# Kernel tuning notes

Hardware: AMD Instinct MI355X
Metric: run time of the kernel (lower is better)

## Reference

```python
import jax, jax.numpy as jnp
import numpy as np

BS = 2
EMBED = 256
NH = 8
NL = 4
NP = 4
HD = EMBED // NH
SHAPES = [(128, 128), (64, 64), (32, 32), (16, 16)]
NQ = sum(h * w for h, w in SHAPES)  # 21760


def setup_inputs() -> dict:
    key = jax.random.key(0)
    ks = jax.random.split(key, 12)
    s = 1.0 / np.sqrt(EMBED)
    return {
        "query": jax.random.normal(ks[0], (BS, NQ, EMBED), jnp.float32),
        "reference_points": jax.random.uniform(ks[1], (BS, NQ, NL, 2), jnp.float32),
        "value": jax.random.normal(ks[2], (BS, NQ, EMBED), jnp.float32),
        "W_off": jax.random.normal(ks[3], (EMBED, NH * NL * NP * 2), jnp.float32) * 0.01,
        "b_off": jax.random.normal(ks[4], (NH * NL * NP * 2,), jnp.float32) * 0.5,
        "W_attn": jax.random.normal(ks[5], (EMBED, NH * NL * NP), jnp.float32) * 0.02,
        "b_attn": jnp.zeros((NH * NL * NP,), jnp.float32),
        "W_v": jax.random.normal(ks[6], (EMBED, EMBED), jnp.float32) * s,
        "b_v": jnp.zeros((EMBED,), jnp.float32),
        "W_out": jax.random.normal(ks[7], (EMBED, EMBED), jnp.float32) * s,
        "b_out": jnp.zeros((EMBED,), jnp.float32),
        "value_spatial_shapes": np.asarray(SHAPES, dtype=np.int64),
    }


def _ms_deform_attn(value, shapes, loc, aw):
    # value: [bs,V,nh,d]; loc: [bs,nq,nh,L,P,2] in [0,1]; aw: [bs,nq,nh,L,P]
    bs, V, nh, d = value.shape
    nq = loc.shape[1]
    out = jnp.zeros((bs, nq, nh, d), value.dtype)
    start = 0
    b_idx = jnp.arange(bs)[:, None, None, None]
    h_idx = jnp.arange(nh)[None, None, :, None]
    for l, (H, W) in enumerate(shapes):
        H, W = int(H), int(W)
        v = value[:, start:start + H * W].reshape(bs, H, W, nh, d)
        start += H * W
        g = 2.0 * loc[:, :, :, l] - 1.0  # [bs,nq,nh,P,2], grid_sample convention
        # align_corners=False pixel coordinates
        x = ((g[..., 0] + 1.0) * W - 1.0) * 0.5
        y = ((g[..., 1] + 1.0) * H - 1.0) * 0.5
        x0 = jnp.floor(x); y0 = jnp.floor(y)
        wx1 = x - x0; wx0 = 1.0 - wx1
        wy1 = y - y0; wy0 = 1.0 - wy1

        def gather(yi, xi):
            inb = (yi >= 0) & (yi < H) & (xi >= 0) & (xi < W)
            yc = jnp.clip(yi, 0, H - 1).astype(jnp.int32)
            xc = jnp.clip(xi, 0, W - 1).astype(jnp.int32)
            vals = v[b_idx, yc, xc, h_idx]  # [bs,nq,nh,P,d]
            return vals * inb[..., None].astype(v.dtype)

        samp = (gather(y0, x0) * (wy0 * wx0)[..., None]
                + gather(y0, x0 + 1) * (wy0 * wx1)[..., None]
                + gather(y0 + 1, x0) * (wy1 * wx0)[..., None]
                + gather(y0 + 1, x0 + 1) * (wy1 * wx1)[..., None])
        out = out + jnp.einsum('bqhpd,bqhp->bqhd', samp, aw[:, :, :, l])
    return out.reshape(bs, nq, nh * d)


def reference(query, reference_points, value, W_off, b_off, W_attn, b_attn,
              W_v, b_v, W_out, b_out, value_spatial_shapes):
    shapes = np.asarray(value_spatial_shapes)  # static [L,2]
    bs, nq, _ = query.shape
    v = (value @ W_v + b_v).reshape(bs, -1, NH, HD)
    off = (query @ W_off + b_off).reshape(bs, nq, NH, NL, NP, 2)
    aw = (query @ W_attn + b_attn).reshape(bs, nq, NH, NL * NP)
    aw = jax.nn.softmax(aw, axis=-1).reshape(bs, nq, NH, NL, NP)
    # offset normalizer: (W,H) per level
    norm = jnp.asarray(shapes[:, ::-1].astype(np.float32))  # [L,2]
    loc = reference_points[:, :, None, :, None, :] + off / norm[None, None, None, :, None, :]
    out = _ms_deform_attn(v, shapes, loc, aw)
    return out @ W_out + b_out
```

## Files before the change

kernel.cpp:

```cpp
#include <hip/hip_runtime.h>
#include <math.h>

#define BS 2
#define NQ 21760
#define V_LEN 21760
#define EMBED 256
#define NH 8
#define NL 4
#define NP 4
#define HD 32

typedef __bf16 bf16;
typedef __bf16 bf16x8 __attribute__((ext_vector_type(8)));
typedef __bf16 bf16x4 __attribute__((ext_vector_type(4)));
typedef float f32x4 __attribute__((ext_vector_type(4)));
typedef float f32x2 __attribute__((ext_vector_type(2)));
typedef unsigned int u32;

#define GLOAD_LDS16(gp, lp_) \
    __builtin_amdgcn_global_load_lds( \
        (const __attribute__((address_space(1))) unsigned int*)(gp), \
        (__attribute__((address_space(3))) unsigned int*)(lp_), 16, 0, 0)

__global__ __launch_bounds__(256) void cast_all(
    const float* __restrict__ W_v, const float* __restrict__ W_off,
    const float* __restrict__ W_attn, const float* __restrict__ W_out,
    const float* __restrict__ b_off, const float* __restrict__ b_attn,
    bf16* __restrict__ WTv, bf16* __restrict__ WToa, bf16* __restrict__ WTu,
    float* __restrict__ bcat)
{
    const int bid = blockIdx.x;
    if (bid == 896) {
        int id = threadIdx.x;
        if (id < 384) bcat[id] = (id < 256) ? b_off[id] : b_attn[id - 256];
        return;
    }
    int id = bid * 256 + threadIdx.x;
    if (id < 65536) {
        int n = id >> 8, k = id & 255;
        WTv[id] = (bf16)W_v[k * 256 + n];
    } else if (id < 131072) {
        int j = id - 65536; int n = j >> 8, k = j & 255;
        WToa[j] = (bf16)W_off[k * 256 + n];
    } else if (id < 163840) {
        int j = id - 131072; int n = j >> 8, k = j & 255;
        WToa[65536 + j] = (bf16)W_attn[k * 128 + n];
    } else {
        int j = id - 163840; int n = j >> 8, k = j & 255;
        WTu[j] = (bf16)W_out[k * 256 + n];
    }
}

template<bool A_F32, bool OUT_BF16>
__global__ __launch_bounds__(256) void gemm_mfma(
    const void* __restrict__ Av, const bf16* __restrict__ WT,
    const float* __restrict__ bias, void* __restrict__ Cv,
    int N, int K, int ntn)
{
    const int bnt = blockIdx.x % ntn;
    const int bmt = blockIdx.x / ntn;
    const int bm = bmt * 128, bn = bnt * 128;

    __shared__ __align__(16) bf16 Bs[2][128 * 32];
    __shared__ __align__(16) unsigned char AsRaw[2][A_F32 ? 128 * 32 * 4
                                                         : 128 * 32 * 2];

    const int tid = threadIdx.x;
    const int lane = tid & 63, wv = tid >> 6;
    const int wr = wv >> 1, wc = wv & 1;
    const int quad = lane >> 4, l16 = lane & 15;

    f32x4 acc[4][4];
    #pragma unroll
    for (int i = 0; i < 4; i++)
        #pragma unroll
        for (int j = 0; j < 4; j++)
            acc[i][j] = (f32x4){0.f, 0.f, 0.f, 0.f};

    const int b_row = tid >> 2, b_chunk = tid & 3;
    const int a_row8 = tid >> 3, a_phys = tid & 7;
    constexpr int NB = A_F32 ? 6 : 4;

    auto stage = [&](int buf, int k0) {
        if constexpr (A_F32) {
            const float* A = (const float*)Av;
            #pragma unroll
            for (int p = 0; p < 4; p++) {
                int row = a_row8 + p * 32;
                int csrc = a_phys ^ (row & 7);
                GLOAD_LDS16(&A[(size_t)(bm + row) * K + k0 + csrc * 4],
                            &AsRaw[buf][p * 4096 + tid * 16]);
            }
        } else {
            const bf16* A = (const bf16*)Av;
            #pragma unroll
            for (int p = 0; p < 2; p++) {
                int row = b_row + p * 64;
                GLOAD_LDS16(&A[(size_t)(bm + row) * K + k0 + b_chunk * 8],
                            &AsRaw[buf][p * 4096 + tid * 16]);
            }
        }
        #pragma unroll
        for (int p = 0; p < 2; p++) {
            int row = b_row + p * 64;
            GLOAD_LDS16(&WT[(size_t)(bn + row) * K + k0 + b_chunk * 8],
                        (unsigned char*)&Bs[buf][0] + p * 4096 + tid * 16);
        }
    };

    const int nt = K >> 5;
    stage(0, 0);
    int cur = 0;
    for (int t = 0; t < nt; t++) {
        __builtin_amdgcn_s_barrier();
        if (t + 1 < nt) {
            stage(cur ^ 1, (t + 1) << 5);
            asm volatile("s_waitcnt vmcnt(%0)" :: "n"(NB) : "memory");
        } else {
            asm volatile("s_waitcnt vmcnt(0)" ::: "memory");
        }
        __builtin_amdgcn_s_barrier();

        bf16x8 af[4], bfr[4];
        if constexpr (A_F32) {
            const float* Asf = (const float*)&AsRaw[cur][0];
            #pragma unroll
            for (int mi = 0; mi < 4; mi++) {
                int r = wr * 64 + mi * 16 + l16;
                int g = r & 7;
                f32x4 u0 = *(const f32x4*)&Asf[r * 32 + ((2 * quad) ^ g) * 4];
                f32x4 u1 = *(const f32x4*)&Asf[r * 32 + ((2 * quad + 1) ^ g) * 4];
                bf16x8 hh;
                hh[0] = (bf16)u0[0]; hh[1] = (bf16)u0[1]; hh[2] = (bf16)u0[2]; hh[3] = (bf16)u0[3];
                hh[4] = (bf16)u1[0]; hh[5] = (bf16)u1[1]; hh[6] = (bf16)u1[2]; hh[7] = (bf16)u1[3];
                af[mi] = hh;
            }
        } else {
            const bf16* Asb = (const bf16*)&AsRaw[cur][0];
            #pragma unroll
            for (int mi = 0; mi < 4; mi++) {
                int r = wr * 64 + mi * 16 + l16;
                af[mi] = *(const bf16x8*)&Asb[r * 32 + quad * 8];
            }
        }
        #pragma unroll
        for (int ni = 0; ni < 4; ni++) {
            int r = wc * 64 + ni * 16 + l16;
            bfr[ni] = *(const bf16x8*)&Bs[cur][r * 32 + quad * 8];
        }
        #pragma unroll
        for (int mi = 0; mi < 4; mi++)
            #pragma unroll
            for (int ni = 0; ni < 4; ni++)
                acc[mi][ni] = __builtin_amdgcn_mfma_f32_16x16x32_bf16(
                    af[mi], bfr[ni], acc[mi][ni], 0, 0, 0);
        cur ^= 1;
    }

    #pragma unroll
    for (int mi = 0; mi < 4; mi++) {
        #pragma unroll
        for (int ni = 0; ni < 4; ni++) {
            const int col = bn + wc * 64 + ni * 16 + l16;
            const int row0 = bm + wr * 64 + mi * 16 + quad * 4;
            const float bc = bias[col];
            #pragma unroll
            for (int r = 0; r < 4; r++) {
                float v = acc[mi][ni][r] + bc;
                if constexpr (OUT_BF16)
                    ((bf16*)Cv)[(size_t)(row0 + r) * N + col] = (bf16)v;
                else
                    ((float*)Cv)[(size_t)(row0 + r) * N + col] = v;
            }
        }
    }
}

__global__ __launch_bounds__(256) void deform_sample(
    const bf16* __restrict__ vproj, const float* __restrict__ offaw,
    const float* __restrict__ refp, bf16* __restrict__ sampled)
{
    const int wv = threadIdx.x >> 6;
    const int t = threadIdx.x & 63;
    const int q = blockIdx.x * 4 + wv;
    const int b = blockIdx.y;
    const int bq = b * NQ + q;

    __shared__ __align__(16) float s_off[4][256];
    __shared__ __align__(16) float s_aw[4][128];
    __shared__ __align__(16) float s_w[4][128][4];
    __shared__ __align__(16) int   s_idx[4][128][4];

    const float* row = offaw + (size_t)bq * 384;
    #pragma unroll
    for (int i = 0; i < 4; i++) {
        int j = t + i * 64;
        s_off[wv][j ^ (((j >> 5) & 7) << 2)] = row[j];
    }
    #pragma unroll
    for (int i = 0; i < 2; i++) s_aw[wv][t + i * 64] = row[256 + t + i * 64];
    __syncthreads();

    {
        const int h = t >> 3, e = t & 7;
        float v0 = s_aw[wv][h * 16 + e];
        float v1 = s_aw[wv][h * 16 + 8 + e];
        float m = fmaxf(v0, v1);
        m = fmaxf(m, __shfl_xor(m, 1));
        m = fmaxf(m, __shfl_xor(m, 2));
        m = fmaxf(m, __shfl_xor(m, 4));
        float e0 = __expf(v0 - m), e1 = __expf(v1 - m);
        float ssum = e0 + e1;
        ssum += __shfl_xor(ssum, 1);
        ssum += __shfl_xor(ssum, 2);
        ssum += __shfl_xor(ssum, 4);
        float rs = 1.0f / ssum;
        s_aw[wv][h * 16 + e] = e0 * rs;
        s_aw[wv][h * 16 + 8 + e] = e1 * rs;
    }
    __syncthreads();

    #pragma unroll
    for (int sI = 0; sI < 2; sI++) {
        int h = t & 7;
        int lp = (t >> 3) + sI * 8;
        int l = lp >> 2, p = lp & 3;
        int Wl = 128 >> l, Hl = 128 >> l;
        int st = (l == 0) ? 0 : (l == 1) ? 16384 : (l == 2) ? 20480 : 21504;
        float rx = refp[((size_t)bq * 4 + l) * 2 + 0];
        float ry = refp[((size_t)bq * 4 + l) * 2 + 1];
        int j = h * 32 + lp * 2;
        float2 oxy = *(const float2*)&s_off[wv][j ^ (h << 2)];
        float ox = oxy.x, oy = oxy.y;
        float fW = (float)Wl, fH = (float)Hl;
        float x = (rx + ox / fW) * fW - 0.5f;
        float y = (ry + oy / fH) * fH - 0.5f;
        float xf = floorf(x), yf = floorf(y);
        int x0 = (int)xf, y0 = (int)yf;
        float wx1 = x - xf, wx0 = 1.f - wx1;
        float wy1 = y - yf, wy0 = 1.f - wy1;
        float aw = s_aw[wv][h * 16 + lp];
        bool vx0 = (x0 >= 0) && (x0 < Wl);
        bool vx1 = (x0 + 1 >= 0) && (x0 + 1 < Wl);
        bool vy0 = (y0 >= 0) && (y0 < Hl);
        bool vy1 = (y0 + 1 >= 0) && (y0 + 1 < Hl);
        int cx0 = min(max(x0, 0), Wl - 1), cx1 = min(max(x0 + 1, 0), Wl - 1);
        int cy0 = min(max(y0, 0), Hl - 1), cy1 = min(max(y0 + 1, 0), Hl - 1);
        int d = lp * 8 + h;
        s_idx[wv][d][0] = st + cy0 * Wl + cx0;  s_w[wv][d][0] = (vy0 && vx0) ? wy0 * wx0 * aw : 0.f;
        s_idx[wv][d][1] = st + cy0 * Wl + cx1;  s_w[wv][d][1] = (vy0 && vx1) ? wy0 * wx1 * aw : 0.f;
        s_idx[wv][d][2] = st + cy1 * Wl + cx0;  s_w[wv][d][2] = (vy1 && vx0) ? wy1 * wx0 * aw : 0.f;
        s_idx[wv][d][3] = st + cy1 * Wl + cx1;  s_w[wv][d][3] = (vy1 && vx1) ? wy1 * wx1 * aw : 0.f;
    }
    __syncthreads();

    const int h = t >> 3;
    const int choff = t * 4;
    const bf16* vbc = vproj + (size_t)b * V_LEN * EMBED + choff;
    f32x2 acc01 = {0.f, 0.f}, acc23 = {0.f, 0.f};
    #pragma unroll 8
    for (int lp = 0; lp < 16; lp++) {
        const int d = lp * 8 + h;
        const float4 w4 = *(const float4*)&s_w[wv][d][0];
        const int4  i4 = *(const int4*)&s_idx[wv][d][0];
        uint2 r0 = *(const uint2*)(vbc + (i4.x << 8));
        uint2 r1 = *(const uint2*)(vbc + (i4.y << 8));
        uint2 r2 = *(const uint2*)(vbc + (i4.z << 8));
        uint2 r3 = *(const uint2*)(vbc + (i4.w << 8));
        f32x2 v;
        v[0] = __uint_as_float(r0.x << 16); v[1] = __uint_as_float(r0.x & 0xFFFF0000u);
        acc01 += v * w4.x;
        v[0] = __uint_as_float(r0.y << 16); v[1] = __uint_as_float(r0.y & 0xFFFF0000u);
        acc23 += v * w4.x;
        v[0] = __uint_as_float(r1.x << 16); v[1] = __uint_as_float(r1.x & 0xFFFF0000u);
        acc01 += v * w4.y;
        v[0] = __uint_as_float(r1.y << 16); v[1] = __uint_as_float(r1.y & 0xFFFF0000u);
        acc23 += v * w4.y;
        v[0] = __uint_as_float(r2.x << 16); v[1] = __uint_as_float(r2.x & 0xFFFF0000u);
        acc01 += v * w4.z;
        v[0] = __uint_as_float(r2.y << 16); v[1] = __uint_as_float(r2.y & 0xFFFF0000u);
        acc23 += v * w4.z;
        v[0] = __uint_as_float(r3.x << 16); v[1] = __uint_as_float(r3.x & 0xFFFF0000u);
        acc01 += v * w4.w;
        v[0] = __uint_as_float(r3.y << 16); v[1] = __uint_as_float(r3.y & 0xFFFF0000u);
        acc23 += v * w4.w;
    }

    bf16x4 o;
    o[0] = (bf16)acc01[0]; o[1] = (bf16)acc01[1];
    o[2] = (bf16)acc23[0]; o[3] = (bf16)acc23[1];
    *(bf16x4*)&sampled[(size_t)bq * 256 + choff] = o;
}

extern "C" void kernel_launch(void* const* d_in, const int* in_sizes, int n_in,
                              void* d_out, int out_size, void* d_ws, size_t ws_size,
                              hipStream_t stream)
{
    const float* query  = (const float*)d_in[0];
    const float* refp   = (const float*)d_in[1];
    const float* value  = (const float*)d_in[2];
    const float* W_off  = (const float*)d_in[3];
    const float* b_off  = (const float*)d_in[4];
    const float* W_attn = (const float*)d_in[5];
    const float* b_attn = (const float*)d_in[6];
    const float* W_v    = (const float*)d_in[7];
    const float* b_v    = (const float*)d_in[8];
    const float* W_out  = (const float*)d_in[9];
    const float* b_out  = (const float*)d_in[10];
    float* out = (float*)d_out;

    const int M = BS * NQ;

    char* ws = (char*)d_ws;
    bf16*  WTv   = (bf16*)ws;                      ws += 256 * 256 * 2;
    bf16*  WToa  = (bf16*)ws;                      ws += 384 * 256 * 2;
    bf16*  WTu   = (bf16*)ws;                      ws += 256 * 256 * 2;
    float* bcat  = (float*)ws;                     ws += 384 * 4;
    bf16*  vproj = (bf16*)ws;                      ws += (size_t)M * 256 * 2;
    float* offaw = (float*)ws;                     ws += (size_t)M * 384 * 4;
    bf16*  samp  = (bf16*)ws;                      ws += (size_t)M * 256 * 2;

    cast_all<<<897, 256, 0, stream>>>(W_v, W_off, W_attn, W_out, b_off, b_attn,
                                      WTv, WToa, WTu, bcat);

    gemm_mfma<true, true><<<(M / 128) * 2, 256, 0, stream>>>(value, WTv, b_v, vproj, 256, 256, 2);
    gemm_mfma<true, false><<<(M / 128) * 3, 256, 0, stream>>>(query, WToa, bcat, offaw, 384, 256, 3);
    deform_sample<<<dim3(NQ / 4, BS), dim3(256), 0, stream>>>(vproj, offaw, refp, samp);
    gemm_mfma<false, false><<<(M / 128) * 2, 256, 0, stream>>>(samp, WTu, b_out, out, 256, 256, 2);
}
```

Baseline: 293.8 us.

## Widen deform gathers to 16B, softmax in registers, tile weight transpose, reorder GEMM blocks

```diff
diff --git a/kernel.cpp b/kernel.cpp
--- a/kernel.cpp
+++ b/kernel.cpp
@@ -30,24 +30,31 @@
     float* __restrict__ bcat)
 {
     const int bid = blockIdx.x;
-    if (bid == 896) {
-        int id = threadIdx.x;
-        if (id < 384) bcat[id] = (id < 256) ? b_off[id] : b_attn[id - 256];
+    const int tid = threadIdx.x;
+    if (bid == 56) {
+        if (tid < 384) bcat[tid] = (tid < 256) ? b_off[tid] : b_attn[tid - 256];
         return;
     }
-    int id = bid * 256 + threadIdx.x;
-    if (id < 65536) {
-        int n = id >> 8, k = id & 255;
-        WTv[id] = (bf16)W_v[k * 256 + n];
-    } else if (id < 131072) {
-        int j = id - 65536; int n = j >> 8, k = j & 255;
-        WToa[j] = (bf16)W_off[k * 256 + n];
-    } else if (id < 163840) {
-        int j = id - 131072; int n = j >> 8, k = j & 255;
-        WToa[65536 + j] = (bf16)W_attn[k * 128 + n];
-    } else {
-        int j = id - 163840; int n = j >> 8, k = j & 255;
-        WTu[j] = (bf16)W_out[k * 256 + n];
+    const float* W; bf16* WT; int N, tile;
+    if (bid < 16)      { W = W_v;    WT = WTv;           N = 256; tile = bid; }
+    else if (bid < 32) { W = W_off;  WT = WToa;          N = 256; tile = bid - 16; }
+    else if (bid < 40) { W = W_attn; WT = WToa + 65536;  N = 128; tile = bid - 32; }
+    else               { W = W_out;  WT = WTu;           N = 256; tile = bid - 40; }
+    const int ntn = N >> 6;
+    const int k0 = (tile / ntn) * 64, n0 = (tile % ntn) * 64;
+
+    __shared__ float lds[64][65];
+    const int c = tid & 63, r4 = tid >> 6;
+    #pragma unroll
+    for (int p = 0; p < 16; p++) {
+        int rr = r4 + p * 4;
+        lds[rr][c] = W[(size_t)(k0 + rr) * N + n0 + c];
+    }
+    __syncthreads();
+    #pragma unroll
+    for (int p = 0; p < 16; p++) {
+        int i = r4 + p * 4;
+        WT[(size_t)(n0 + i) * 256 + k0 + c] = (bf16)lds[c][i];
     }
 }
 
@@ -57,8 +64,9 @@
     const float* __restrict__ bias, void* __restrict__ Cv,
     int N, int K, int ntn)
 {
-    const int bnt = blockIdx.x % ntn;
-    const int bmt = blockIdx.x / ntn;
+    const int nmt = gridDim.x / ntn;
+    const int bmt = blockIdx.x % nmt;
+    const int bnt = blockIdx.x / nmt;
     const int bm = bmt * 128, bn = bnt * 128;
 
     __shared__ __align__(16) bf16 Bs[2][128 * 32];
@@ -186,67 +194,49 @@
     const int b = blockIdx.y;
     const int bq = b * NQ + q;
 
-    __shared__ __align__(16) float s_off[4][256];
-    __shared__ __align__(16) float s_aw[4][128];
     __shared__ __align__(16) float s_w[4][128][4];
     __shared__ __align__(16) int   s_idx[4][128][4];
 
     const float* row = offaw + (size_t)bq * 384;
-    #pragma unroll
-    for (int i = 0; i < 4; i++) {
-        int j = t + i * 64;
-        s_off[wv][j ^ (((j >> 5) & 7) << 2)] = row[j];
-    }
-    #pragma unroll
-    for (int i = 0; i < 2; i++) s_aw[wv][t + i * 64] = row[256 + t + i * 64];
-    __syncthreads();
-
-    {
-        const int h = t >> 3, e = t & 7;
-        float v0 = s_aw[wv][h * 16 + e];
-        float v1 = s_aw[wv][h * 16 + 8 + e];
-        float m = fmaxf(v0, v1);
-        m = fmaxf(m, __shfl_xor(m, 1));
-        m = fmaxf(m, __shfl_xor(m, 2));
-        m = fmaxf(m, __shfl_xor(m, 4));
-        float e0 = __expf(v0 - m), e1 = __expf(v1 - m);
-        float ssum = e0 + e1;
-        ssum += __shfl_xor(ssum, 1);
-        ssum += __shfl_xor(ssum, 2);
-        ssum += __shfl_xor(ssum, 4);
-        float rs = 1.0f / ssum;
-        s_aw[wv][h * 16 + e] = e0 * rs;
-        s_aw[wv][h * 16 + 8 + e] = e1 * rs;
-    }
-    __syncthreads();
+
+    const int hp = t & 7, e = t >> 3;
+    float l0 = row[256 + hp * 16 + e];
+    float l1 = row[256 + hp * 16 + e + 8];
+    float m = fmaxf(l0, l1);
+    m = fmaxf(m, __shfl_xor(m, 8));
+    m = fmaxf(m, __shfl_xor(m, 16));
+    m = fmaxf(m, __shfl_xor(m, 32));
+    float e0 = __expf(l0 - m), e1 = __expf(l1 - m);
+    float ssum = e0 + e1;
+    ssum += __shfl_xor(ssum, 8);
+    ssum += __shfl_xor(ssum, 16);
+    ssum += __shfl_xor(ssum, 32);
+    float rs = 1.0f / ssum;
+    float awv[2] = {e0 * rs, e1 * rs};
 
     #pragma unroll
     for (int sI = 0; sI < 2; sI++) {
-        int h = t & 7;
-        int lp = (t >> 3) + sI * 8;
-        int l = lp >> 2, p = lp & 3;
+        int lp = e + sI * 8;
+        int l = lp >> 2;
         int Wl = 128 >> l, Hl = 128 >> l;
         int st = (l == 0) ? 0 : (l == 1) ? 16384 : (l == 2) ? 20480 : 21504;
-        float rx = refp[((size_t)bq * 4 + l) * 2 + 0];
-        float ry = refp[((size_t)bq * 4 + l) * 2 + 1];
-        int j = h * 32 + lp * 2;
-        float2 oxy = *(const float2*)&s_off[wv][j ^ (h << 2)];
-        float ox = oxy.x, oy = oxy.y;
+        float2 rp = *(const float2*)&refp[((size_t)bq * 4 + l) * 2];
+        float2 oxy = *(const float2*)&row[hp * 32 + lp * 2];
         float fW = (float)Wl, fH = (float)Hl;
-        float x = (rx + ox / fW) * fW - 0.5f;
-        float y = (ry + oy / fH) * fH - 0.5f;
+        float x = (rp.x + oxy.x / fW) * fW - 0.5f;
+        float y = (rp.y + oxy.y / fH) * fH - 0.5f;
         float xf = floorf(x), yf = floorf(y);
         int x0 = (int)xf, y0 = (int)yf;
         float wx1 = x - xf, wx0 = 1.f - wx1;
         float wy1 = y - yf, wy0 = 1.f - wy1;
-        float aw = s_aw[wv][h * 16 + lp];
+        float aw = awv[sI];
         bool vx0 = (x0 >= 0) && (x0 < Wl);
         bool vx1 = (x0 + 1 >= 0) && (x0 + 1 < Wl);
         bool vy0 = (y0 >= 0) && (y0 < Hl);
         bool vy1 = (y0 + 1 >= 0) && (y0 + 1 < Hl);
         int cx0 = min(max(x0, 0), Wl - 1), cx1 = min(max(x0 + 1, 0), Wl - 1);
         int cy0 = min(max(y0, 0), Hl - 1), cy1 = min(max(y0 + 1, 0), Hl - 1);
-        int d = lp * 8 + h;
+        int d = lp * 8 + hp;
         s_idx[wv][d][0] = st + cy0 * Wl + cx0;  s_w[wv][d][0] = (vy0 && vx0) ? wy0 * wx0 * aw : 0.f;
         s_idx[wv][d][1] = st + cy0 * Wl + cx1;  s_w[wv][d][1] = (vy0 && vx1) ? wy0 * wx1 * aw : 0.f;
         s_idx[wv][d][2] = st + cy1 * Wl + cx0;  s_w[wv][d][2] = (vy1 && vx0) ? wy1 * wx0 * aw : 0.f;
@@ -254,42 +244,45 @@
     }
     __syncthreads();
 
-    const int h = t >> 3;
-    const int choff = t * 4;
+    const int half = t >> 5;
+    const int hg = (t & 31) >> 2;
+    const int cg = t & 3;
+    const int choff = hg * 32 + cg * 8;
     const bf16* vbc = vproj + (size_t)b * V_LEN * EMBED + choff;
-    f32x2 acc01 = {0.f, 0.f}, acc23 = {0.f, 0.f};
-    #pragma unroll 8
-    for (int lp = 0; lp < 16; lp++) {
-        const int d = lp * 8 + h;
+
+    f32x2 a01 = {0.f, 0.f}, a23 = {0.f, 0.f}, a45 = {0.f, 0.f}, a67 = {0.f, 0.f};
+    #pragma unroll
+    for (int lpp = 0; lpp < 8; lpp++) {
+        const int d = (lpp + 8 * half) * 8 + hg;
         const float4 w4 = *(const float4*)&s_w[wv][d][0];
         const int4  i4 = *(const int4*)&s_idx[wv][d][0];
-        uint2 r0 = *(const uint2*)(vbc + (i4.x << 8));
-        uint2 r1 = *(const uint2*)(vbc + (i4.y << 8));
-        uint2 r2 = *(const uint2*)(vbc + (i4.z << 8));
-        uint2 r3 = *(const uint2*)(vbc + (i4.w << 8));
+        uint4 r0 = *(const uint4*)(vbc + ((size_t)i4.x << 8));
+        uint4 r1 = *(const uint4*)(vbc + ((size_t)i4.y << 8));
+        uint4 r2 = *(const uint4*)(vbc + ((size_t)i4.z << 8));
+        uint4 r3 = *(const uint4*)(vbc + ((size_t)i4.w << 8));
         f32x2 v;
-        v[0] = __uint_as_float(r0.x << 16); v[1] = __uint_as_float(r0.x & 0xFFFF0000u);
-        acc01 += v * w4.x;
-        v[0] = __uint_as_float(r0.y << 16); v[1] = __uint_as_float(r0.y & 0xFFFF0000u);
-        acc23 += v * w4.x;
-        v[0] = __uint_as_float(r1.x << 16); v[1] = __uint_as_float(r1.x & 0xFFFF0000u);
-        acc01 += v * w4.y;
-        v[0] = __uint_as_float(r1.y << 16); v[1] = __uint_as_float(r1.y & 0xFFFF0000u);
-        acc23 += v * w4.y;
-        v[0] = __uint_as_float(r2.x << 16); v[1] = __uint_as_float(r2.x & 0xFFFF0000u);
-        acc01 += v * w4.z;
-        v[0] = __uint_as_float(r2.y << 16); v[1] = __uint_as_float(r2.y & 0xFFFF0000u);
-        acc23 += v * w4.z;
-        v[0] = __uint_as_float(r3.x << 16); v[1] = __uint_as_float(r3.x & 0xFFFF0000u);
-        acc01 += v * w4.w;
-        v[0] = __uint_as_float(r3.y << 16); v[1] = __uint_as_float(r3.y & 0xFFFF0000u);
-        acc23 += v * w4.w;
-    }
-
-    bf16x4 o;
-    o[0] = (bf16)acc01[0]; o[1] = (bf16)acc01[1];
-    o[2] = (bf16)acc23[0]; o[3] = (bf16)acc23[1];
-    *(bf16x4*)&sampled[(size_t)bq * 256 + choff] = o;
+        #define ACC8(rr, ww) \
+            v[0] = __uint_as_float((rr).x << 16); v[1] = __uint_as_float((rr).x & 0xFFFF0000u); a01 += v * (ww); \
+            v[0] = __uint_as_float((rr).y << 16); v[1] = __uint_as_float((rr).y & 0xFFFF0000u); a23 += v * (ww); \
+            v[0] = __uint_as_float((rr).z << 16); v[1] = __uint_as_float((rr).z & 0xFFFF0000u); a45 += v * (ww); \
+            v[0] = __uint_as_float((rr).w << 16); v[1] = __uint_as_float((rr).w & 0xFFFF0000u); a67 += v * (ww);
+        ACC8(r0, w4.x)
+        ACC8(r1, w4.y)
+        ACC8(r2, w4.z)
+        ACC8(r3, w4.w)
+        #undef ACC8
+    }
+
+    float s[8] = {a01[0], a01[1], a23[0], a23[1], a45[0], a45[1], a67[0], a67[1]};
+    #pragma unroll
+    for (int i = 0; i < 8; i++) s[i] += __shfl_xor(s[i], 32);
+
+    if (t < 32) {
+        bf16x8 o;
+        #pragma unroll
+        for (int i = 0; i < 8; i++) o[i] = (bf16)s[i];
+        *(bf16x8*)&sampled[(size_t)bq * 256 + choff] = o;
+    }
 }
 
 extern "C" void kernel_launch(void* const* d_in, const int* in_sizes, int n_in,
@@ -320,8 +313,8 @@
     float* offaw = (float*)ws;                     ws += (size_t)M * 384 * 4;
     bf16*  samp  = (bf16*)ws;                      ws += (size_t)M * 256 * 2;
 
-    cast_all<<<897, 256, 0, stream>>>(W_v, W_off, W_attn, W_out, b_off, b_attn,
-                                      WTv, WToa, WTu, bcat);
+    cast_all<<<57, 256, 0, stream>>>(W_v, W_off, W_attn, W_out, b_off, b_attn,
+                                     WTv, WToa, WTu, bcat);
 
     gemm_mfma<true, true><<<(M / 128) * 2, 256, 0, stream>>>(value, WTv, b_v, vproj, 256, 256, 2);
     gemm_mfma<true, false><<<(M / 128) * 3, 256, 0, stream>>>(query, WToa, bcat, offaw, 384, 256, 3);
```

New measurement: 293.3 us. No clear change (-0.2%).
